# Performance work log

Measured on AMD Instinct MI355X. Metric: run time of the kernel, lower is better.

## Reference

```python
import jax, jax.numpy as jnp
import numpy as np

B, S, D, H = 4, 2048, 1024, 16
HD = D // H  # head_dim = 64

def setup_inputs() -> dict:
    key = jax.random.key(0)
    ks = jax.random.split(key, 6)
    scale = 1.0 / np.sqrt(D)
    x = jax.random.normal(ks[0], (B, S, D), dtype=jnp.float32)
    Wq = jax.random.normal(ks[1], (D, D), dtype=jnp.float32) * scale
    Wk = jax.random.normal(ks[2], (D, D), dtype=jnp.float32) * scale
    Wv = jax.random.normal(ks[3], (D, D), dtype=jnp.float32) * scale
    Wo = jax.random.normal(ks[4], (D, D), dtype=jnp.float32) * scale
    z = jnp.zeros((D,), dtype=jnp.float32)
    return {"x": x, "Wq": Wq, "bq": z, "Wk": Wk, "bk": z, "Wv": Wv, "bv": z, "Wo": Wo, "bo": z}

def reference(x, Wq, bq, Wk, bk, Wv, bv, Wo, bo):
    b, s, d = x.shape
    hd = d // H
    def split_heads(t):
        return t.reshape(b, s, H, hd).swapaxes(1, 2)  # [B,H,S,hd]
    q = split_heads(x @ Wq + bq)
    k = split_heads(x @ Wk + bk)
    v = split_heads(x @ Wv + bv)
    logits = jnp.einsum('bhqd,bhkd->bhqk', q, k) / jnp.sqrt(jnp.asarray(hd, x.dtype))
    attn = jax.nn.softmax(logits, axis=-1)
    vals = jnp.einsum('bhqk,bhkd->bhqd', attn, v)
    vals = vals.swapaxes(1, 2).reshape(b, s, d)
    return vals @ Wo + bo
```

## Files before the change

### kernel.cpp

```cpp
#include <hip/hip_runtime.h>
#include <hip/hip_bf16.h>
#include <cstdint>
#include <cstddef>


typedef __attribute__((ext_vector_type(8))) short short8;
typedef __attribute__((ext_vector_type(4))) short short4v;
typedef __attribute__((ext_vector_type(8))) unsigned short ushort8;
typedef __attribute__((ext_vector_type(4))) unsigned short ushort4v;
typedef __attribute__((ext_vector_type(4))) float floatx4;

#define LOG2E 1.44269504088896340736f
#define QSCALE (0.125f * LOG2E)

__device__ __forceinline__ floatx4 mfma16bf(short4v a, short4v b, floatx4 c) {
#if __HIP_DEVICE_COMPILE__
  return __builtin_amdgcn_mfma_f32_16x16x16bf16_1k(a, b, c, 0, 0, 0);
#else
  (void)a; (void)b;
  return c;
#endif
}

__device__ __forceinline__ unsigned short f2bf(float f) {
  union { float f; unsigned int u; } c; c.f = f;
  return (unsigned short)((c.u + 0x7fffu + ((c.u >> 16) & 1u)) >> 16);
}

__device__ __forceinline__ unsigned int pack_bf16(float a, float b) {
  unsigned int ua = __builtin_bit_cast(unsigned int, a) + 0x8000u;
  unsigned int ub = __builtin_bit_cast(unsigned int, b) + 0x8000u;
  return __builtin_amdgcn_perm(ub, ua, 0x07060302);
}

__device__ __forceinline__ void gl_lds16(const void* g, void* l) {
  __builtin_amdgcn_global_load_lds((__attribute__((address_space(1))) void*)g,
                                   (__attribute__((address_space(3))) void*)l, 16, 0, 0);
}

__global__ __launch_bounds__(256) void cast_x_kernel(const float* __restrict__ x,
                                                     unsigned short* __restrict__ xb, int n4) {
  int i = blockIdx.x * 256 + threadIdx.x;
  if (i >= n4) return;
  float4 v = ((const float4*)x)[i];
  ushort4v o;
  o.x = f2bf(v.x); o.y = f2bf(v.y); o.z = f2bf(v.z); o.w = f2bf(v.w);
  ((ushort4v*)xb)[i] = o;
}

__global__ __launch_bounds__(256) void transpose_w_kernel(
    const float* __restrict__ Wq, const float* __restrict__ Wk,
    const float* __restrict__ Wv, const float* __restrict__ Wo,
    unsigned short* __restrict__ Wqkv_t, unsigned short* __restrict__ Wo_t) {
  __shared__ float tile[32][33];
  const int which = blockIdx.z;
  const float* src = (which == 0) ? Wq : (which == 1) ? Wk : (which == 2) ? Wv : Wo;
  unsigned short* dst = (which == 3) ? Wo_t : (Wqkv_t + (size_t)which * 1024 * 1024);
  const int bn = blockIdx.x * 32;
  const int bk = blockIdx.y * 32;
  const int tx = threadIdx.x & 31, ty = threadIdx.x >> 5;
#pragma unroll
  for (int r = 0; r < 32; r += 8)
    tile[ty + r][tx] = src[(size_t)(bk + ty + r) * 1024 + bn + tx];
  __syncthreads();
#pragma unroll
  for (int r = 0; r < 32; r += 8)
    dst[(size_t)(bn + ty + r) * 1024 + bk + tx] = f2bf(tile[tx][ty + r]);
}

template <int MODE>
__global__ __launch_bounds__(256, 3) void gemm_bt(
    const unsigned short* __restrict__ A, const unsigned short* __restrict__ Bt,
    int M, int N, int K,
    const float* __restrict__ bias0, const float* __restrict__ bias1,
    const float* __restrict__ bias2,
    unsigned short* __restrict__ outQ, unsigned short* __restrict__ outK,
    unsigned short* __restrict__ outVt, float* __restrict__ outF) {
  __shared__ unsigned short As[128 * 32];
  __shared__ unsigned short Bs[128 * 32];

  const int tid = threadIdx.x;
  const int lane = tid & 63;
  const int wid = tid >> 6;
  const int wm = wid >> 1, wn = wid & 1;
  const int l15 = lane & 15, q4 = lane >> 4;
  const int bm = blockIdx.x * 128, bn = blockIdx.y * 128;

  const int rowL = lane >> 2;
  const int segL = (lane & 3) * 16;

  const char* Ab = (const char*)A;
  const char* Bb = (const char*)Bt;
  const size_t strideA = (size_t)K * 2;

  floatx4 acc[4][4] = {};

  for (int k0 = 0; k0 < K; k0 += 32) {
    __syncthreads();
#pragma unroll
    for (int c0 = 0; c0 < 2; ++c0) {
      const int c = wid * 2 + c0;
      gl_lds16(Ab + (size_t)(bm + c * 16 + rowL) * strideA + (size_t)k0 * 2 + segL,
               &As[c * 512]);
      gl_lds16(Bb + (size_t)(bn + c * 16 + rowL) * strideA + (size_t)k0 * 2 + segL,
               &Bs[c * 512]);
    }
    __syncthreads();

    short8 af[4], bfr[4];
#pragma unroll
    for (int i = 0; i < 4; ++i)
      af[i] = *(const short8*)&As[(wm * 64 + i * 16 + l15) * 32 + q4 * 8];
#pragma unroll
    for (int j = 0; j < 4; ++j)
      bfr[j] = *(const short8*)&Bs[(wn * 64 + j * 16 + l15) * 32 + q4 * 8];
#pragma unroll
    for (int i = 0; i < 4; ++i)
#pragma unroll
      for (int j = 0; j < 4; ++j)
        acc[i][j] = __builtin_amdgcn_mfma_f32_16x16x32_bf16(af[i], bfr[j], acc[i][j], 0, 0, 0);
  }

#pragma unroll
  for (int i = 0; i < 4; ++i) {
    const int row0 = bm + wm * 64 + i * 16 + q4 * 4;
#pragma unroll
    for (int j = 0; j < 4; ++j) {
      const int gn = bn + wn * 64 + j * 16 + l15;
      if (MODE == 0) {
        const int b = row0 >> 11, s0 = row0 & 2047;
        const int region = gn >> 10, d = gn & 1023;
        const int h = d >> 6, hd = d & 63;
        const size_t bh = (size_t)(b * 16 + h);
        if (region == 0) {
          const float bb = bias0[d];
#pragma unroll
          for (int r = 0; r < 4; ++r)
            outQ[(bh * 2048 + s0 + r) * 64 + hd] = f2bf((acc[i][j][r] + bb) * QSCALE);
        } else if (region == 1) {
          const float bb = bias1[d];
#pragma unroll
          for (int r = 0; r < 4; ++r)
            outK[(bh * 2048 + s0 + r) * 64 + hd] = f2bf(acc[i][j][r] + bb);
        } else {
          const float bb = bias2[d];
          ushort4v pk;
#pragma unroll
          for (int r = 0; r < 4; ++r) pk[r] = f2bf(acc[i][j][r] + bb);
          *(ushort4v*)&outVt[(bh * 64 + hd) * 2048 + s0] = pk;
        }
      } else {
        const float bb = bias0[gn];
#pragma unroll
        for (int r = 0; r < 4; ++r)
          outF[(size_t)(row0 + r) * N + gn] = acc[i][j][r] + bb;
      }
    }
  }
}

__global__ __launch_bounds__(256, 4) void flash_attn(
    const unsigned short* __restrict__ Q, const unsigned short* __restrict__ Kg,
    const unsigned short* __restrict__ Vt, unsigned short* __restrict__ Oout) {
  __shared__ unsigned short Ks[64 * 72];
  __shared__ unsigned short Vs[64 * 72];

  const int tid = threadIdx.x, lane = tid & 63, wid = tid >> 6;
  const int l15 = lane & 15, q4 = lane >> 4;
  const int bh = blockIdx.y;
  const int bb = bh >> 4, hh = bh & 15;
  const int q0 = blockIdx.x * 64;
  const size_t base = (size_t)bh * 2048 * 64;

  const unsigned short* qrow = Q + base + (size_t)(q0 + wid * 16 + l15) * 64;
  const short8 qf0 = *(const short8*)(qrow + q4 * 8);
  const short8 qf1 = *(const short8*)(qrow + 32 + q4 * 8);

  const int sr = tid >> 2;
  const int sg = (tid & 3) * 16;
  const int ks4 = (sg >> 4) * 4;

  ushort8 kr0, kr1, vr0, vr1;
  {
    const unsigned short* gk = Kg + base + (size_t)sr * 64 + sg;
    kr0 = *(const ushort8*)gk; kr1 = *(const ushort8*)(gk + 8);
    const unsigned short* gv = Vt + base + (size_t)sr * 2048 + sg;
    vr0 = *(const ushort8*)gv; vr1 = *(const ushort8*)(gv + 8);
  }

  floatx4 oacc[4] = {};
  float l_lane = 0.0f;

  for (int kb = 0; kb < 2048; kb += 64) {
    if (kb) __syncthreads();
    *(ushort8*)&Ks[sr * 72 + sg] = kr0;
    *(ushort8*)&Ks[sr * 72 + sg + 8] = kr1;
    *(ushort4v*)&Vs[sr * 72 + ks4]      = __builtin_shufflevector(vr0, vr0, 0, 1, 2, 3);
    *(ushort4v*)&Vs[sr * 72 + 16 + ks4] = __builtin_shufflevector(vr0, vr0, 4, 5, 6, 7);
    *(ushort4v*)&Vs[sr * 72 + 32 + ks4] = __builtin_shufflevector(vr1, vr1, 0, 1, 2, 3);
    *(ushort4v*)&Vs[sr * 72 + 48 + ks4] = __builtin_shufflevector(vr1, vr1, 4, 5, 6, 7);
    __syncthreads();

    if (kb + 64 < 2048) {
      const unsigned short* gk = Kg + base + (size_t)(kb + 64 + sr) * 64 + sg;
      kr0 = *(const ushort8*)gk; kr1 = *(const ushort8*)(gk + 8);
      const unsigned short* gv = Vt + base + (size_t)sr * 2048 + (kb + 64) + sg;
      vr0 = *(const ushort8*)gv; vr1 = *(const ushort8*)(gv + 8);
    }

    floatx4 sacc[4] = {};
#pragma unroll
    for (int t = 0; t < 4; ++t) {
      const unsigned short* krow = &Ks[(t * 16 + l15) * 72];
      short8 kf0 = *(const short8*)(krow + q4 * 8);
      short8 kf1 = *(const short8*)(krow + 32 + q4 * 8);
      sacc[t] = __builtin_amdgcn_mfma_f32_16x16x32_bf16(kf0, qf0, sacc[t], 0, 0, 0);
      sacc[t] = __builtin_amdgcn_mfma_f32_16x16x32_bf16(kf1, qf1, sacc[t], 0, 0, 0);
    }

    short4v pf[4];
#pragma unroll
    for (int t = 0; t < 4; ++t) {
      float p0 = exp2f(sacc[t][0]), p1 = exp2f(sacc[t][1]);
      float p2 = exp2f(sacc[t][2]), p3 = exp2f(sacc[t][3]);
      l_lane += (p0 + p1) + (p2 + p3);
      union { unsigned int u[2]; short4v s; } cv;
      cv.u[0] = pack_bf16(p0, p1);
      cv.u[1] = pack_bf16(p2, p3);
      pf[t] = cv.s;
    }

#pragma unroll
    for (int t = 0; t < 4; ++t) {
      const unsigned short* vrow = &Vs[(t * 16 + l15) * 72 + q4 * 16];
      short8 v01 = *(const short8*)vrow;
      short8 v23 = *(const short8*)(vrow + 8);
      oacc[t] = mfma16bf(__builtin_shufflevector(v01, v01, 0, 1, 2, 3), pf[0], oacc[t]);
      oacc[t] = mfma16bf(__builtin_shufflevector(v01, v01, 4, 5, 6, 7), pf[1], oacc[t]);
      oacc[t] = mfma16bf(__builtin_shufflevector(v23, v23, 0, 1, 2, 3), pf[2], oacc[t]);
      oacc[t] = mfma16bf(__builtin_shufflevector(v23, v23, 4, 5, 6, 7), pf[3], oacc[t]);
    }
  }

  l_lane += __shfl_xor(l_lane, 16);
  l_lane += __shfl_xor(l_lane, 32);
  const float inv = 1.0f / l_lane;
  const int s = q0 + wid * 16 + l15;
  unsigned short* orow = Oout + ((size_t)bb * 2048 + s) * 1024 + hh * 64;
#pragma unroll
  for (int t = 0; t < 4; ++t) {
    union { unsigned int u[2]; ushort4v s4; } cv;
    cv.u[0] = pack_bf16(oacc[t][0] * inv, oacc[t][1] * inv);
    cv.u[1] = pack_bf16(oacc[t][2] * inv, oacc[t][3] * inv);
    *(ushort4v*)(orow + t * 16 + q4 * 4) = cv.s4;
  }
}

extern "C" void kernel_launch(void* const* d_in, const int* in_sizes, int n_in,
                              void* d_out, int out_size, void* d_ws, size_t ws_size,
                              hipStream_t stream) {
  const float* x  = (const float*)d_in[0];
  const float* Wq = (const float*)d_in[1];
  const float* bq = (const float*)d_in[2];
  const float* Wk = (const float*)d_in[3];
  const float* bk = (const float*)d_in[4];
  const float* Wv = (const float*)d_in[5];
  const float* bv = (const float*)d_in[6];
  const float* Wo = (const float*)d_in[7];
  const float* bo = (const float*)d_in[8];
  float* out = (float*)d_out;

  char* ws = (char*)d_ws;
  unsigned short* xb     = (unsigned short*)(ws);
  unsigned short* wqkv_t = (unsigned short*)(ws + (16u << 20));
  unsigned short* wo_t   = (unsigned short*)(ws + (22u << 20));
  unsigned short* Qb     = (unsigned short*)(ws + (24u << 20));
  unsigned short* Kb     = (unsigned short*)(ws + (40u << 20));
  unsigned short* Vtb    = (unsigned short*)(ws + (56u << 20));
  unsigned short* attn   = (unsigned short*)(ws + (72u << 20));
  (void)in_sizes; (void)n_in; (void)out_size; (void)ws_size;

  cast_x_kernel<<<dim3(8192), 256, 0, stream>>>(x, xb, 8192 * 1024 / 4);
  transpose_w_kernel<<<dim3(32, 32, 4), 256, 0, stream>>>(Wq, Wk, Wv, Wo, wqkv_t, wo_t);
  gemm_bt<0><<<dim3(64, 24), 256, 0, stream>>>(xb, wqkv_t, 8192, 3072, 1024,
                                               bq, bk, bv, Qb, Kb, Vtb, nullptr);
  flash_attn<<<dim3(32, 64), 256, 0, stream>>>(Qb, Kb, Vtb, attn);
  gemm_bt<1><<<dim3(64, 8), 256, 0, stream>>>(attn, wo_t, 8192, 1024, 1024,
                                              bo, nullptr, nullptr,
                                              nullptr, nullptr, nullptr, out);
}
```

Baseline: 321.9 us.

## Process two query tiles per block with double-buffered K/V and 16x16x32 PV MFMA

```diff
diff --git a/kernel.cpp b/kernel.cpp
--- a/kernel.cpp
+++ b/kernel.cpp
@@ -5,22 +5,12 @@
 
 
 typedef __attribute__((ext_vector_type(8))) short short8;
-typedef __attribute__((ext_vector_type(4))) short short4v;
 typedef __attribute__((ext_vector_type(8))) unsigned short ushort8;
 typedef __attribute__((ext_vector_type(4))) unsigned short ushort4v;
 typedef __attribute__((ext_vector_type(4))) float floatx4;
 
 #define LOG2E 1.44269504088896340736f
 #define QSCALE (0.125f * LOG2E)
-
-__device__ __forceinline__ floatx4 mfma16bf(short4v a, short4v b, floatx4 c) {
-#if __HIP_DEVICE_COMPILE__
-  return __builtin_amdgcn_mfma_f32_16x16x16bf16_1k(a, b, c, 0, 0, 0);
-#else
-  (void)a; (void)b;
-  return c;
-#endif
-}
 
 __device__ __forceinline__ unsigned short f2bf(float f) {
   union { float f; unsigned int u; } c; c.f = f;
@@ -159,100 +149,124 @@
   }
 }
 
-__global__ __launch_bounds__(256, 4) void flash_attn(
+__global__ __launch_bounds__(256, 3) void flash_attn(
     const unsigned short* __restrict__ Q, const unsigned short* __restrict__ Kg,
     const unsigned short* __restrict__ Vt, unsigned short* __restrict__ Oout) {
-  __shared__ unsigned short Ks[64 * 72];
-  __shared__ unsigned short Vs[64 * 72];
+  __shared__ unsigned short Ks[2][64 * 72];
+  __shared__ unsigned short Vs[2][64 * 72];
 
   const int tid = threadIdx.x, lane = tid & 63, wid = tid >> 6;
   const int l15 = lane & 15, q4 = lane >> 4;
   const int bh = blockIdx.y;
   const int bb = bh >> 4, hh = bh & 15;
-  const int q0 = blockIdx.x * 64;
+  const int q0 = blockIdx.x * 128;
   const size_t base = (size_t)bh * 2048 * 64;
 
-  const unsigned short* qrow = Q + base + (size_t)(q0 + wid * 16 + l15) * 64;
-  const short8 qf0 = *(const short8*)(qrow + q4 * 8);
-  const short8 qf1 = *(const short8*)(qrow + 32 + q4 * 8);
+  const unsigned short* qrowA = Q + base + (size_t)(q0 + wid * 16 + l15) * 64;
+  const unsigned short* qrowB = qrowA + 64 * 64;
+  const short8 qa0 = *(const short8*)(qrowA + q4 * 8);
+  const short8 qa1 = *(const short8*)(qrowA + 32 + q4 * 8);
+  const short8 qb0 = *(const short8*)(qrowB + q4 * 8);
+  const short8 qb1 = *(const short8*)(qrowB + 32 + q4 * 8);
 
   const int sr = tid >> 2;
   const int sg = (tid & 3) * 16;
-  const int ks4 = (sg >> 4) * 4;
+  const int loc = sr & 31;
+  const int ph = (loc >> 4) & 1, pq = (loc >> 2) & 3, pr = loc & 3;
+  const int gp = (sr & 32) + pq * 8 + ph * 4 + pr;
+  const unsigned short* Kbase = Kg + base + (size_t)gp * 64 + sg;
+  const unsigned short* Vbase = Vt + base + (size_t)sr * 2048 + sg;
 
   ushort8 kr0, kr1, vr0, vr1;
-  {
-    const unsigned short* gk = Kg + base + (size_t)sr * 64 + sg;
-    kr0 = *(const ushort8*)gk; kr1 = *(const ushort8*)(gk + 8);
-    const unsigned short* gv = Vt + base + (size_t)sr * 2048 + sg;
-    vr0 = *(const ushort8*)gv; vr1 = *(const ushort8*)(gv + 8);
-  }
-
-  floatx4 oacc[4] = {};
-  float l_lane = 0.0f;
-
-  for (int kb = 0; kb < 2048; kb += 64) {
-    if (kb) __syncthreads();
-    *(ushort8*)&Ks[sr * 72 + sg] = kr0;
-    *(ushort8*)&Ks[sr * 72 + sg + 8] = kr1;
-    *(ushort4v*)&Vs[sr * 72 + ks4]      = __builtin_shufflevector(vr0, vr0, 0, 1, 2, 3);
-    *(ushort4v*)&Vs[sr * 72 + 16 + ks4] = __builtin_shufflevector(vr0, vr0, 4, 5, 6, 7);
-    *(ushort4v*)&Vs[sr * 72 + 32 + ks4] = __builtin_shufflevector(vr1, vr1, 0, 1, 2, 3);
-    *(ushort4v*)&Vs[sr * 72 + 48 + ks4] = __builtin_shufflevector(vr1, vr1, 4, 5, 6, 7);
+  kr0 = *(const ushort8*)Kbase;       kr1 = *(const ushort8*)(Kbase + 8);
+  vr0 = *(const ushort8*)Vbase;       vr1 = *(const ushort8*)(Vbase + 8);
+  *(ushort8*)&Ks[0][sr * 72 + sg] = kr0;  *(ushort8*)&Ks[0][sr * 72 + sg + 8] = kr1;
+  *(ushort8*)&Vs[0][sr * 72 + sg] = vr0;  *(ushort8*)&Vs[0][sr * 72 + sg + 8] = vr1;
+  kr0 = *(const ushort8*)(Kbase + 4096);  kr1 = *(const ushort8*)(Kbase + 4104);
+  vr0 = *(const ushort8*)(Vbase + 64);    vr1 = *(const ushort8*)(Vbase + 72);
+
+  floatx4 oaccA[4] = {}, oaccB[4] = {};
+  float lA = 0.0f, lB = 0.0f;
+
+  for (int it = 0; it < 32; ++it) {
+    const int cur = it & 1;
     __syncthreads();
-
-    if (kb + 64 < 2048) {
-      const unsigned short* gk = Kg + base + (size_t)(kb + 64 + sr) * 64 + sg;
-      kr0 = *(const ushort8*)gk; kr1 = *(const ushort8*)(gk + 8);
-      const unsigned short* gv = Vt + base + (size_t)sr * 2048 + (kb + 64) + sg;
-      vr0 = *(const ushort8*)gv; vr1 = *(const ushort8*)(gv + 8);
-    }
-
-    floatx4 sacc[4] = {};
+    if (it < 31) {
+      *(ushort8*)&Ks[cur ^ 1][sr * 72 + sg] = kr0;
+      *(ushort8*)&Ks[cur ^ 1][sr * 72 + sg + 8] = kr1;
+      *(ushort8*)&Vs[cur ^ 1][sr * 72 + sg] = vr0;
+      *(ushort8*)&Vs[cur ^ 1][sr * 72 + sg + 8] = vr1;
+    }
+    if (it < 30) {
+      const unsigned short* kp = Kbase + (size_t)(it + 2) * 4096;
+      const unsigned short* vp = Vbase + (size_t)(it + 2) * 64;
+      kr0 = *(const ushort8*)kp;       kr1 = *(const ushort8*)(kp + 8);
+      vr0 = *(const ushort8*)vp;       vr1 = *(const ushort8*)(vp + 8);
+    }
+
+    floatx4 sA[4] = {}, sB[4] = {};
 #pragma unroll
     for (int t = 0; t < 4; ++t) {
-      const unsigned short* krow = &Ks[(t * 16 + l15) * 72];
+      const unsigned short* krow = &Ks[cur][(t * 16 + l15) * 72];
       short8 kf0 = *(const short8*)(krow + q4 * 8);
       short8 kf1 = *(const short8*)(krow + 32 + q4 * 8);
-      sacc[t] = __builtin_amdgcn_mfma_f32_16x16x32_bf16(kf0, qf0, sacc[t], 0, 0, 0);
-      sacc[t] = __builtin_amdgcn_mfma_f32_16x16x32_bf16(kf1, qf1, sacc[t], 0, 0, 0);
-    }
-
-    short4v pf[4];
+      sA[t] = __builtin_amdgcn_mfma_f32_16x16x32_bf16(kf0, qa0, sA[t], 0, 0, 0);
+      sA[t] = __builtin_amdgcn_mfma_f32_16x16x32_bf16(kf1, qa1, sA[t], 0, 0, 0);
+      sB[t] = __builtin_amdgcn_mfma_f32_16x16x32_bf16(kf0, qb0, sB[t], 0, 0, 0);
+      sB[t] = __builtin_amdgcn_mfma_f32_16x16x32_bf16(kf1, qb1, sB[t], 0, 0, 0);
+    }
+
+    short8 pA[2], pB[2];
+#pragma unroll
+    for (int c = 0; c < 2; ++c) {
+      float ea0 = exp2f(sA[2 * c][0]), ea1 = exp2f(sA[2 * c][1]);
+      float ea2 = exp2f(sA[2 * c][2]), ea3 = exp2f(sA[2 * c][3]);
+      float ea4 = exp2f(sA[2 * c + 1][0]), ea5 = exp2f(sA[2 * c + 1][1]);
+      float ea6 = exp2f(sA[2 * c + 1][2]), ea7 = exp2f(sA[2 * c + 1][3]);
+      lA += ((ea0 + ea1) + (ea2 + ea3)) + ((ea4 + ea5) + (ea6 + ea7));
+      union { unsigned int u[4]; short8 s; } ca;
+      ca.u[0] = pack_bf16(ea0, ea1); ca.u[1] = pack_bf16(ea2, ea3);
+      ca.u[2] = pack_bf16(ea4, ea5); ca.u[3] = pack_bf16(ea6, ea7);
+      pA[c] = ca.s;
+      float eb0 = exp2f(sB[2 * c][0]), eb1 = exp2f(sB[2 * c][1]);
+      float eb2 = exp2f(sB[2 * c][2]), eb3 = exp2f(sB[2 * c][3]);
+      float eb4 = exp2f(sB[2 * c + 1][0]), eb5 = exp2f(sB[2 * c + 1][1]);
+      float eb6 = exp2f(sB[2 * c + 1][2]), eb7 = exp2f(sB[2 * c + 1][3]);
+      lB += ((eb0 + eb1) + (eb2 + eb3)) + ((eb4 + eb5) + (eb6 + eb7));
+      union { unsigned int u[4]; short8 s; } cb;
+      cb.u[0] = pack_bf16(eb0, eb1); cb.u[1] = pack_bf16(eb2, eb3);
+      cb.u[2] = pack_bf16(eb4, eb5); cb.u[3] = pack_bf16(eb6, eb7);
+      pB[c] = cb.s;
+    }
+
 #pragma unroll
     for (int t = 0; t < 4; ++t) {
-      float p0 = exp2f(sacc[t][0]), p1 = exp2f(sacc[t][1]);
-      float p2 = exp2f(sacc[t][2]), p3 = exp2f(sacc[t][3]);
-      l_lane += (p0 + p1) + (p2 + p3);
-      union { unsigned int u[2]; short4v s; } cv;
-      cv.u[0] = pack_bf16(p0, p1);
-      cv.u[1] = pack_bf16(p2, p3);
-      pf[t] = cv.s;
-    }
-
-#pragma unroll
-    for (int t = 0; t < 4; ++t) {
-      const unsigned short* vrow = &Vs[(t * 16 + l15) * 72 + q4 * 16];
-      short8 v01 = *(const short8*)vrow;
-      short8 v23 = *(const short8*)(vrow + 8);
-      oacc[t] = mfma16bf(__builtin_shufflevector(v01, v01, 0, 1, 2, 3), pf[0], oacc[t]);
-      oacc[t] = mfma16bf(__builtin_shufflevector(v01, v01, 4, 5, 6, 7), pf[1], oacc[t]);
-      oacc[t] = mfma16bf(__builtin_shufflevector(v23, v23, 0, 1, 2, 3), pf[2], oacc[t]);
-      oacc[t] = mfma16bf(__builtin_shufflevector(v23, v23, 4, 5, 6, 7), pf[3], oacc[t]);
+      const unsigned short* vrow = &Vs[cur][(t * 16 + l15) * 72 + q4 * 8];
+      short8 vf0 = *(const short8*)vrow;
+      short8 vf1 = *(const short8*)(vrow + 32);
+      oaccA[t] = __builtin_amdgcn_mfma_f32_16x16x32_bf16(vf0, pA[0], oaccA[t], 0, 0, 0);
+      oaccA[t] = __builtin_amdgcn_mfma_f32_16x16x32_bf16(vf1, pA[1], oaccA[t], 0, 0, 0);
+      oaccB[t] = __builtin_amdgcn_mfma_f32_16x16x32_bf16(vf0, pB[0], oaccB[t], 0, 0, 0);
+      oaccB[t] = __builtin_amdgcn_mfma_f32_16x16x32_bf16(vf1, pB[1], oaccB[t], 0, 0, 0);
     }
   }
 
-  l_lane += __shfl_xor(l_lane, 16);
-  l_lane += __shfl_xor(l_lane, 32);
-  const float inv = 1.0f / l_lane;
-  const int s = q0 + wid * 16 + l15;
-  unsigned short* orow = Oout + ((size_t)bb * 2048 + s) * 1024 + hh * 64;
+  lA += __shfl_xor(lA, 16); lA += __shfl_xor(lA, 32);
+  lB += __shfl_xor(lB, 16); lB += __shfl_xor(lB, 32);
+  const float invA = 1.0f / lA, invB = 1.0f / lB;
+  const int sA_row = q0 + wid * 16 + l15;
+  unsigned short* orowA = Oout + ((size_t)bb * 2048 + sA_row) * 1024 + hh * 64;
+  unsigned short* orowB = orowA + (size_t)64 * 1024;
 #pragma unroll
   for (int t = 0; t < 4; ++t) {
-    union { unsigned int u[2]; ushort4v s4; } cv;
-    cv.u[0] = pack_bf16(oacc[t][0] * inv, oacc[t][1] * inv);
-    cv.u[1] = pack_bf16(oacc[t][2] * inv, oacc[t][3] * inv);
-    *(ushort4v*)(orow + t * 16 + q4 * 4) = cv.s4;
+    union { unsigned int u[2]; ushort4v s4; } cva;
+    cva.u[0] = pack_bf16(oaccA[t][0] * invA, oaccA[t][1] * invA);
+    cva.u[1] = pack_bf16(oaccA[t][2] * invA, oaccA[t][3] * invA);
+    *(ushort4v*)(orowA + t * 16 + q4 * 4) = cva.s4;
+    union { unsigned int u[2]; ushort4v s4; } cvb;
+    cvb.u[0] = pack_bf16(oaccB[t][0] * invB, oaccB[t][1] * invB);
+    cvb.u[1] = pack_bf16(oaccB[t][2] * invB, oaccB[t][3] * invB);
+    *(ushort4v*)(orowB + t * 16 + q4 * 4) = cvb.s4;
   }
 }
 
@@ -284,7 +298,7 @@
   transpose_w_kernel<<<dim3(32, 32, 4), 256, 0, stream>>>(Wq, Wk, Wv, Wo, wqkv_t, wo_t);
   gemm_bt<0><<<dim3(64, 24), 256, 0, stream>>>(xb, wqkv_t, 8192, 3072, 1024,
                                                bq, bk, bv, Qb, Kb, Vtb, nullptr);
-  flash_attn<<<dim3(32, 64), 256, 0, stream>>>(Qb, Kb, Vtb, attn);
+  flash_attn<<<dim3(16, 64), 256, 0, stream>>>(Qb, Kb, Vtb, attn);
   gemm_bt<1><<<dim3(64, 8), 256, 0, stream>>>(attn, wo_t, 8192, 1024, 1024,
                                               bo, nullptr, nullptr,
                                               nullptr, nullptr, nullptr, out);
```

Measured after the change: 296.1 us. 8.0% less time.
